# Kernel optimization log

Hardware: AMD Instinct MI355X
Metric: run time of the kernel (lower is better)

The kernel has to match this reference:

```python
import jax, jax.numpy as jnp
import numpy as np


def _maxpool2x2(x):
    # x: [N, C, H, W] -> [N, C, H//2, W//2]
    return jax.lax.reduce_window(x, -jnp.inf, jax.lax.max,
                                 (1, 1, 2, 2), (1, 1, 2, 2), 'VALID')


def _head(a, W1, b1, W2, b2, W3, b3):
    # headModel: maxpool -> (adaptive avgpool to 7x7 is identity here) -> flatten -> classifier (eval mode)
    mp = _maxpool2x2(a)                      # [N, 512, 7, 7]
    flat = mp.reshape(mp.shape[0], -1)       # [N, 25088]
    h = jax.nn.relu(flat @ W1.T + b1)        # [N, 4096]
    h = jax.nn.relu(h @ W2.T + b2)           # [N, 4096]
    return h @ W3.T + b3                     # [N, 1000]


def setup_inputs() -> dict:
    key = jax.random.key(0)
    ks = jax.random.split(key, 7)
    C, HW, FC, NC = 512, 14, 4096, 1000
    acts = jax.random.uniform(ks[0], (1, C, HW, HW), dtype=jnp.float32)  # post-ReLU feature map
    s1 = 1.0 / np.sqrt(C * 7 * 7)
    s2 = 1.0 / np.sqrt(FC)
    return {
        'activations': acts,
        'W1': jax.random.normal(ks[1], (FC, C * 7 * 7), dtype=jnp.float32) * s1,
        'b1': jax.random.normal(ks[2], (FC,), dtype=jnp.float32) * 0.01,
        'W2': jax.random.normal(ks[3], (FC, FC), dtype=jnp.float32) * s2,
        'b2': jax.random.normal(ks[4], (FC,), dtype=jnp.float32) * 0.01,
        'W3': jax.random.normal(ks[5], (NC, FC), dtype=jnp.float32) * s2,
        'b3': jax.random.normal(ks[6], (NC,), dtype=jnp.float32) * 0.01,
        'ht': 224,
        'wt': 224,
    }


def reference(activations, W1, b1, W2, b2, W3, b3, ht, wt):
    C = activations.shape[1]
    logits = _head(activations, W1, b1, W2, b2, W3, b3)   # [1, 1000]
    img_class = jnp.argmax(logits[0])
    base = logits[0, img_class]

    # Batch all C channel ablations: abl[i] = activations with channel i zeroed.
    mask = (1.0 - jnp.eye(C, dtype=activations.dtype))[:, :, None, None]  # [C, C, 1, 1]
    abl = activations * mask                                              # [C, C, 14, 14]
    logits_new = _head(abl, W1, b1, W2, b2, W3, b3)                        # [C, 1000]
    alpha = (base - jnp.take(logits_new, img_class, axis=1)) / base        # [C]

    # fused = relu(sum_i alpha_i * bilinear_resize(act_i)); resize is linear,
    # so weight in activation space and do one resize (same math as the loop).
    weighted = jnp.einsum('c,chw->hw', alpha, activations[0])              # [14, 14]
    sal = jax.image.resize(weighted[None, None], (1, 1, ht, wt),
                           method='bilinear')[0, 0]                        # [ht, wt]
    fused = jax.nn.relu(sal)
    mn, mx = fused.min(), fused.max()
    denom = jnp.where(mx != mn, mx - mn, 1.0)
    fused = jnp.where(mx != mn, (fused - mn) / denom, fused)
    return fused, img_class
```

## Files before the change

kernel.cpp:

```cpp
#include <hip/hip_runtime.h>
#include <math.h>

#define CCH 512
#define F1 25088
#define FC 4096
#define NCLS 1000
#define OW 224
#define KSPLIT 4
#define KSLICE 1024
#define PSTRIDE (CCH*FC)

#define WS_DT 0
#define WS_MP (WS_DT + FC*CCH)
#define WS_H1PRE (WS_MP + F1)
#define WS_H1 (WS_H1PRE + FC)
#define WS_H2 (WS_H1 + FC)
#define WS_H2PART (WS_H2 + FC)
#define WS_LOGITS (WS_H2PART + 4*FC)
#define WS_CLSBASE (WS_LOGITS + NCLS)
#define WS_ALPHA (WS_CLSBASE + 2)
#define WS_MINMAX (WS_ALPHA + CCH)
#define WS_LOGPART (WS_MINMAX + 2)
#define WS_A (WS_LOGPART + 64*CCH)
#define WS_PARTB (WS_A + CCH*FC/2)
#define WS_END (WS_PARTB + KSPLIT*CCH*FC/2)
#define WS_NEED_BYTES ((size_t)WS_END * 4)

typedef __attribute__((ext_vector_type(8))) short bfrag;
typedef __attribute__((ext_vector_type(4))) float f32x4;

static __device__ __forceinline__ unsigned short f2bf(float x) {
    unsigned u = __float_as_uint(x);
    unsigned r = 0x7FFFu + ((u >> 16) & 1u);
    return (unsigned short)((u + r) >> 16);
}

#define GLD16(g, l) __builtin_amdgcn_global_load_lds( \
    (const __attribute__((address_space(1))) void*)(g), \
    (__attribute__((address_space(3))) void*)(l), 16, 0, 0)

__global__ void k_maxpool(const float* __restrict__ act, float* __restrict__ ws) {
    int t = threadIdx.x;
    if (blockIdx.x == 0) {
        if (t == 0) ((int*)(ws + WS_MINMAX))[0] = 0x7F800000;
        if (t == 1) ((int*)(ws + WS_MINMAX))[1] = 0;
    }
    int idx = blockIdx.x * 256 + t;
    if (idx >= CCH * 49) return;
    int c = idx / 49, r = idx % 49, y = r / 7, x = r % 7;
    const float* a = act + c * 196 + (2 * y) * 14 + 2 * x;
    float m = fmaxf(fmaxf(a[0], a[1]), fmaxf(a[14], a[15]));
    ws[WS_MP + idx] = m;
}

__global__ __launch_bounds__(256) void k_phi5(const float* __restrict__ W1,
                                              const float* __restrict__ mp,
                                              const float* __restrict__ b1,
                                              float* __restrict__ Dt,
                                              float* __restrict__ h1pre,
                                              float* __restrict__ h1) {
    __shared__ float buf[12544];
    __shared__ float red[256];
    int j = blockIdx.x, t = threadIdx.x;
    const float* row = W1 + (size_t)j * F1;
    float sh[2];
    #pragma unroll
    for (int h = 0; h < 2; ++h) {
        __syncthreads();
        const float4* src = (const float4*)(row + h * 12544);
        const float4* msc = (const float4*)(mp + h * 12544);
        for (int n = t; n < 3136; n += 256) {
            float4 w = src[n], m = msc[n];
            float4 p;
            p.x = w.x * m.x; p.y = w.y * m.y; p.z = w.z * m.z; p.w = w.w * m.w;
            *(float4*)&buf[n * 4] = p;
        }
        __syncthreads();
        const float* bb = buf + t * 49;
        float s = 0.f;
        #pragma unroll
        for (int k = 0; k < 49; ++k) s += bb[k];
        Dt[(size_t)j * CCH + h * 256 + t] = s;
        sh[h] = s;
    }
    red[t] = sh[0] + sh[1];
    __syncthreads();
    if (t < 128) red[t] += red[t + 128];
    __syncthreads();
    if (t < 64) {
        float v = red[t] + red[t + 64];
        for (int off = 32; off > 0; off >>= 1) v += __shfl_down(v, off, 64);
        if (t == 0) { float hv = b1[j] + v; h1pre[j] = hv; h1[j] = fmaxf(hv, 0.f); }
    }
}

template <bool RELU>
__global__ void k_gemv4096(const float* __restrict__ M, const float* __restrict__ v,
                           const float* __restrict__ bias, float* __restrict__ out) {
    int j = blockIdx.x, t = threadIdx.x;
    const float4* row = (const float4*)(M + (size_t)j * FC);
    const float4* vv = (const float4*)v;
    float s = 0.f;
    #pragma unroll
    for (int q = 0; q < 4; ++q) {
        int n = q * 256 + t;
        float4 w = row[n], x = vv[n];
        s += w.x * x.x + w.y * x.y + w.z * x.z + w.w * x.w;
    }
    __shared__ float red[256];
    red[t] = s; __syncthreads();
    if (t < 128) red[t] += red[t + 128]; __syncthreads();
    if (t < 64)  red[t] += red[t + 64];  __syncthreads();
    if (t < 64) {
        float x = red[t];
        for (int off = 32; off > 0; off >>= 1) x += __shfl_down(x, off, 64);
        if (t == 0) { float r = bias[j] + x; out[j] = RELU ? fmaxf(r, 0.f) : r; }
    }
}

__global__ void k_argmax(const float* __restrict__ logits, float* __restrict__ clsbase,
                         float* __restrict__ dout_cls) {
    int t = threadIdx.x;
    float best = -INFINITY; int bi = NCLS;
    for (int n = t; n < NCLS; n += 256) {
        float v = logits[n];
        if (v > best || (v == best && n < bi)) { best = v; bi = n; }
    }
    __shared__ float bv[256]; __shared__ int bidx[256];
    bv[t] = best; bidx[t] = bi; __syncthreads();
    for (int o = 128; o > 0; o >>= 1) {
        if (t < o) {
            float v2 = bv[t + o]; int i2 = bidx[t + o];
            if (v2 > bv[t] || (v2 == bv[t] && i2 < bidx[t])) { bv[t] = v2; bidx[t] = i2; }
        }
        __syncthreads();
    }
    if (t == 0) { clsbase[0] = (float)bidx[0]; clsbase[1] = bv[0]; *dout_cls = (float)bidx[0]; }
}

__global__ __launch_bounds__(256) void k_abuild(const float* __restrict__ Dt,
                                                const float* __restrict__ h1pre,
                                                unsigned short* __restrict__ A) {
    __shared__ unsigned short tile[64][72];
    int kt = blockIdx.x, it = blockIdx.y, t = threadIdx.x;
    int k0 = kt * 64, i0 = it * 64;
    #pragma unroll
    for (int q = 0; q < 16; ++q) {
        int kk = q * 4 + (t >> 6);
        int ii = t & 63;
        float v = fmaxf(h1pre[k0 + kk] - Dt[(size_t)(k0 + kk) * CCH + i0 + ii], 0.f);
        tile[kk][ii] = f2bf(v);
    }
    __syncthreads();
    #pragma unroll
    for (int q = 0; q < 4; ++q) {
        int c = q * 256 + t;
        int ii = c >> 4, kc = c & 15;
        ushort4 v;
        v.x = tile[kc * 4 + 0][ii]; v.y = tile[kc * 4 + 1][ii];
        v.z = tile[kc * 4 + 2][ii]; v.w = tile[kc * 4 + 3][ii];
        *(ushort4*)&A[(size_t)(i0 + ii) * FC + k0 + kc * 4] = v;
    }
}

__global__ __launch_bounds__(256) void k_mfma_v4(
    const unsigned short* __restrict__ A, const float* __restrict__ W2,
    const float* __restrict__ h1, unsigned short* __restrict__ partb,
    float* __restrict__ h2part) {
    __shared__ char As[16384];
    __shared__ char Bs[16384];
    __shared__ float h1s[KSLICE];
    int nj = blockIdx.x;
    int mi = blockIdx.y;
    int ks = blockIdx.z;
    int t = threadIdx.x;
    int wid = t >> 6, lane = t & 63, lr = lane & 15, lh = lane >> 4;
    int i0 = mi * 128, j0 = nj * 128;
    int wr = (wid >> 1) * 64;
    int wc = (wid & 1) * 64;

    {
        float4 v = *(const float4*)(h1 + ks * KSLICE + t * 4);
        *(float4*)&h1s[t * 4] = v;
    }

    bool doh = (mi == 0);
    float hacc[4] = {0.f, 0.f, 0.f, 0.f};
    f32x4 acc[4][4];
    #pragma unroll
    for (int f = 0; f < 4; ++f)
        #pragma unroll
        for (int n = 0; n < 4; ++n) acc[f][n] = (f32x4){0.f, 0.f, 0.f, 0.f};

    for (int kst = 0; kst < KSLICE; kst += 64) {
        int k0 = ks * KSLICE + kst;
        __syncthreads();
        #pragma unroll
        for (int r = 0; r < 4; ++r) {
            int c = t + 256 * r;
            int row = c >> 3, ch = c & 7;
            GLD16(A + (size_t)(i0 + row) * FC + k0 + ((ch ^ (row & 7)) * 8),
                  As + (size_t)c * 16);
        }
        #pragma unroll
        for (int r = 0; r < 4; ++r) {
            int c = t + 256 * r;
            int row = c >> 3, ch = c & 7;
            int ko = (ch ^ (row & 7)) * 8;
            const float* wp = W2 + (size_t)(j0 + row) * FC + k0 + ko;
            float4 wa = *(const float4*)wp;
            float4 wb = *(const float4*)(wp + 4);
            if (doh) {
                hacc[r] += wa.x * h1s[kst + ko + 0] + wa.y * h1s[kst + ko + 1]
                         + wa.z * h1s[kst + ko + 2] + wa.w * h1s[kst + ko + 3]
                         + wb.x * h1s[kst + ko + 4] + wb.y * h1s[kst + ko + 5]
                         + wb.z * h1s[kst + ko + 6] + wb.w * h1s[kst + ko + 7];
            }
            union { bfrag v; unsigned short u[8]; } pk;
            pk.u[0] = f2bf(wa.x); pk.u[1] = f2bf(wa.y);
            pk.u[2] = f2bf(wa.z); pk.u[3] = f2bf(wa.w);
            pk.u[4] = f2bf(wb.x); pk.u[5] = f2bf(wb.y);
            pk.u[6] = f2bf(wb.z); pk.u[7] = f2bf(wb.w);
            *(bfrag*)(Bs + (size_t)c * 16) = pk.v;
        }
        __syncthreads();
        #pragma unroll
        for (int kf = 0; kf < 2; ++kf) {
            bfrag bv[4];
            #pragma unroll
            for (int n = 0; n < 4; ++n) {
                int br = wc + n * 16 + lr;
                bv[n] = *(const bfrag*)(Bs + ((size_t)br * 8 + ((kf * 4 + lh) ^ (br & 7))) * 16);
            }
            #pragma unroll
            for (int f = 0; f < 4; ++f) {
                int ar = wr + f * 16 + lr;
                bfrag av = *(const bfrag*)(As + ((size_t)ar * 8 + ((kf * 4 + lh) ^ (ar & 7))) * 16);
                #pragma unroll
                for (int n = 0; n < 4; ++n)
                    acc[f][n] = __builtin_amdgcn_mfma_f32_16x16x32_bf16(av, bv[n], acc[f][n], 0, 0, 0);
            }
        }
    }

    if (doh) {
        #pragma unroll
        for (int r = 0; r < 4; ++r) {
            float v = hacc[r];
            v += __shfl_down(v, 4, 8);
            v += __shfl_down(v, 2, 8);
            v += __shfl_down(v, 1, 8);
            if ((t & 7) == 0) h2part[ks * FC + j0 + r * 32 + (t >> 3)] = v;
        }
    }
    unsigned short* pb = partb + (size_t)ks * PSTRIDE;
    #pragma unroll
    for (int f = 0; f < 4; ++f) {
        int row0 = i0 + wr + f * 16 + lh * 4;
        #pragma unroll
        for (int rr = 0; rr < 4; ++rr) {
            #pragma unroll
            for (int n = 0; n < 4; ++n)
                pb[(size_t)(row0 + rr) * FC + j0 + wc + n * 16 + lr] = f2bf(acc[f][n][rr]);
        }
    }
}

__global__ void k_h2sum(const float* __restrict__ h2part, const float* __restrict__ b2,
                        float* __restrict__ h2) {
    int j = blockIdx.x * 256 + threadIdx.x;
    if (j < FC) {
        float v = b2[j] + ((h2part[j] + h2part[FC + j]) + (h2part[2 * FC + j] + h2part[3 * FC + j]));
        h2[j] = fmaxf(v, 0.f);
    }
}

__global__ __launch_bounds__(256) void k_alpha_b(
    const unsigned short* __restrict__ partb, const float* __restrict__ b2,
    const float* __restrict__ W3, const float* __restrict__ b3,
    const float* __restrict__ clsbase, float* __restrict__ alpha) {
    int i = blockIdx.x, t = threadIdx.x;
    int cls = (int)clsbase[0]; float base = clsbase[1];
    const float* w3r = W3 + (size_t)cls * FC;
    float s = 0.f;
    #pragma unroll
    for (int q = 0; q < 2; ++q) {
        int j = (q * 256 + t) * 8;
        uint4 p0 = *(const uint4*)(partb + (size_t)i * FC + j);
        uint4 p1 = *(const uint4*)(partb + (size_t)PSTRIDE + (size_t)i * FC + j);
        uint4 p2 = *(const uint4*)(partb + 2 * (size_t)PSTRIDE + (size_t)i * FC + j);
        uint4 p3 = *(const uint4*)(partb + 3 * (size_t)PSTRIDE + (size_t)i * FC + j);
        #pragma unroll
        for (int e = 0; e < 4; ++e) {
            unsigned a0 = ((const unsigned*)&p0)[e], a1 = ((const unsigned*)&p1)[e];
            unsigned a2 = ((const unsigned*)&p2)[e], a3 = ((const unsigned*)&p3)[e];
            float lo = (__uint_as_float(a0 << 16) + __uint_as_float(a1 << 16))
                     + (__uint_as_float(a2 << 16) + __uint_as_float(a3 << 16));
            float hi = (__uint_as_float(a0 & 0xFFFF0000u) + __uint_as_float(a1 & 0xFFFF0000u))
                     + (__uint_as_float(a2 & 0xFFFF0000u) + __uint_as_float(a3 & 0xFFFF0000u));
            int jj = j + e * 2;
            s += fmaxf(lo + b2[jj], 0.f) * w3r[jj];
            s += fmaxf(hi + b2[jj + 1], 0.f) * w3r[jj + 1];
        }
    }
    __shared__ float red[256];
    red[t] = s; __syncthreads();
    if (t < 128) red[t] += red[t + 128]; __syncthreads();
    if (t < 64)  red[t] += red[t + 64];  __syncthreads();
    if (t < 64) {
        float x = red[t];
        for (int off = 32; off > 0; off >>= 1) x += __shfl_down(x, off, 64);
        if (t == 0) alpha[i] = (base - (x + b3[cls])) / base;
    }
}

__global__ __launch_bounds__(256) void k_gemm_abl(
    const float* __restrict__ Dt, const float* __restrict__ h1pre,
    const float* __restrict__ W2, const float* __restrict__ b2,
    const float* __restrict__ W3, const float* __restrict__ clsbase,
    float* __restrict__ logit_part) {
    int mi = blockIdx.x, nj = blockIdx.y, t = threadIdx.x;
    int tx = t & 15, ty = t >> 4;
    int i0 = mi * 64, j0 = nj * 64;
    __shared__ float As2[16][64];
    __shared__ float Bs2[16][65];
    float acc[4][4] = {};
    for (int k0 = 0; k0 < FC; k0 += 16) {
        #pragma unroll
        for (int r = 0; r < 4; ++r) {
            int e = t + 256 * r; int kk = e >> 6, ii = e & 63;
            As2[kk][ii] = fmaxf(h1pre[k0 + kk] - Dt[(size_t)(k0 + kk) * CCH + i0 + ii], 0.f);
        }
        {
            int jj = t >> 2, kks = (t & 3) * 4;
            const float4 wv = *(const float4*)(W2 + (size_t)(j0 + jj) * FC + k0 + kks);
            Bs2[kks + 0][jj] = wv.x; Bs2[kks + 1][jj] = wv.y;
            Bs2[kks + 2][jj] = wv.z; Bs2[kks + 3][jj] = wv.w;
        }
        __syncthreads();
        #pragma unroll
        for (int kk = 0; kk < 16; ++kk) {
            float4 a4 = *(const float4*)&As2[kk][tx * 4];
            float av[4] = {a4.x, a4.y, a4.z, a4.w};
            float bv[4] = {Bs2[kk][ty * 4 + 0], Bs2[kk][ty * 4 + 1],
                           Bs2[kk][ty * 4 + 2], Bs2[kk][ty * 4 + 3]};
            #pragma unroll
            for (int a = 0; a < 4; ++a)
                #pragma unroll
                for (int b = 0; b < 4; ++b)
                    acc[a][b] = fmaf(av[a], bv[b], acc[a][b]);
        }
        __syncthreads();
    }
    int cls = (int)clsbase[0];
    const float* w3r = W3 + (size_t)cls * FC;
    float prt[4] = {0.f, 0.f, 0.f, 0.f};
    #pragma unroll
    for (int b = 0; b < 4; ++b) {
        int j2 = j0 + ty * 4 + b;
        float bb = b2[j2], w3 = w3r[j2];
        #pragma unroll
        for (int a = 0; a < 4; ++a) prt[a] = fmaf(fmaxf(acc[a][b] + bb, 0.f), w3, prt[a]);
    }
    __shared__ float red2[16][68];
    #pragma unroll
    for (int a = 0; a < 4; ++a) red2[ty][tx * 4 + a] = prt[a];
    __syncthreads();
    if (t < 64) {
        float s = 0.f;
        #pragma unroll
        for (int q = 0; q < 16; ++q) s += red2[q][t];
        logit_part[nj * CCH + i0 + t] = s;
    }
}

__global__ void k_alpha_fb(const float* __restrict__ logit_part, const float* __restrict__ b3,
                           const float* __restrict__ clsbase, float* __restrict__ alpha) {
    int t = blockIdx.x * 256 + threadIdx.x;
    if (t >= CCH) return;
    int cls = (int)clsbase[0]; float base = clsbase[1];
    float s = 0.f;
    for (int q = 0; q < 64; ++q) s += logit_part[q * CCH + t];
    alpha[t] = (base - (s + b3[cls])) / base;
}

__global__ void k_resize2(const float* __restrict__ alpha, const float* __restrict__ act,
                          float* __restrict__ out, int* __restrict__ minmax) {
    __shared__ float sA[CCH];
    __shared__ float sW[196];
    int t = threadIdx.x;
    for (int i = t; i < CCH; i += 256) sA[i] = alpha[i];
    __syncthreads();
    if (t < 196) {
        float s = 0.f;
        for (int c = 0; c < CCH; ++c) s = fmaf(sA[c], act[c * 196 + t], s);
        sW[t] = s;
    }
    __syncthreads();
    int pix = blockIdx.x * 256 + t;
    int y = pix / OW, x = pix % OW;
    float uy = (y + 0.5f) * 0.0625f - 0.5f;
    float ux = (x + 0.5f) * 0.0625f - 0.5f;
    float y0f = floorf(uy), x0f = floorf(ux);
    float fy = uy - y0f, fx = ux - x0f;
    int y0 = (int)y0f, x0 = (int)x0f;
    int y0c = min(max(y0, 0), 13), y1c = min(max(y0 + 1, 0), 13);
    int x0c = min(max(x0, 0), 13), x1c = min(max(x0 + 1, 0), 13);
    float v00 = sW[y0c * 14 + x0c], v01 = sW[y0c * 14 + x1c];
    float v10 = sW[y1c * 14 + x0c], v11 = sW[y1c * 14 + x1c];
    float v0 = v00 + (v01 - v00) * fx;
    float v1 = v10 + (v11 - v10) * fx;
    float v = v0 + (v1 - v0) * fy;
    float f = fmaxf(v, 0.f);
    out[pix] = f;
    __shared__ float rmn[256], rmx[256];
    rmn[t] = f; rmx[t] = f; __syncthreads();
    for (int o = 128; o > 0; o >>= 1) {
        if (t < o) { rmn[t] = fminf(rmn[t], rmn[t + o]); rmx[t] = fmaxf(rmx[t], rmx[t + o]); }
        __syncthreads();
    }
    if (t == 0) {
        atomicMin(&minmax[0], __float_as_int(rmn[0]));
        atomicMax(&minmax[1], __float_as_int(rmx[0]));
    }
}

__global__ void k_norm(float* __restrict__ out, const int* __restrict__ minmax) {
    float mn = __int_as_float(minmax[0]);
    float mx = __int_as_float(minmax[1]);
    int pix = blockIdx.x * 256 + threadIdx.x;
    if (mx != mn) out[pix] = (out[pix] - mn) / (mx - mn);
}

extern "C" void kernel_launch(void* const* d_in, const int* in_sizes, int n_in,
                              void* d_out, int out_size, void* d_ws, size_t ws_size,
                              hipStream_t stream) {
    const float* act = (const float*)d_in[0];
    const float* W1  = (const float*)d_in[1];
    const float* b1  = (const float*)d_in[2];
    const float* W2  = (const float*)d_in[3];
    const float* b2  = (const float*)d_in[4];
    const float* W3  = (const float*)d_in[5];
    const float* b3  = (const float*)d_in[6];
    float* out = (float*)d_out;
    float* ws = (float*)d_ws;
    const bool fast = (ws_size >= WS_NEED_BYTES);

    k_maxpool<<<98, 256, 0, stream>>>(act, ws);
    k_phi5<<<4096, 256, 0, stream>>>(W1, ws + WS_MP, b1, ws + WS_DT,
                                     ws + WS_H1PRE, ws + WS_H1);
    if (fast) {
        k_abuild<<<dim3(64, 8), 256, 0, stream>>>(ws + WS_DT, ws + WS_H1PRE,
                                                  (unsigned short*)(ws + WS_A));
        k_mfma_v4<<<dim3(32, 4, 4), 256, 0, stream>>>(
            (const unsigned short*)(ws + WS_A), W2, ws + WS_H1,
            (unsigned short*)(ws + WS_PARTB), ws + WS_H2PART);
        k_h2sum<<<16, 256, 0, stream>>>(ws + WS_H2PART, b2, ws + WS_H2);
        k_gemv4096<false><<<1000, 256, 0, stream>>>(W3, ws + WS_H2, b3, ws + WS_LOGITS);
        k_argmax<<<1, 256, 0, stream>>>(ws + WS_LOGITS, ws + WS_CLSBASE, out + 50176);
        k_alpha_b<<<CCH, 256, 0, stream>>>((const unsigned short*)(ws + WS_PARTB), b2,
                                           W3, b3, ws + WS_CLSBASE, ws + WS_ALPHA);
    } else {
        k_gemv4096<true><<<4096, 256, 0, stream>>>(W2, ws + WS_H1, b2, ws + WS_H2);
        k_gemv4096<false><<<1000, 256, 0, stream>>>(W3, ws + WS_H2, b3, ws + WS_LOGITS);
        k_argmax<<<1, 256, 0, stream>>>(ws + WS_LOGITS, ws + WS_CLSBASE, out + 50176);
        k_gemm_abl<<<dim3(8, 64), 256, 0, stream>>>(ws + WS_DT, ws + WS_H1PRE, W2, b2, W3,
                                                    ws + WS_CLSBASE, ws + WS_LOGPART);
        k_alpha_fb<<<2, 256, 0, stream>>>(ws + WS_LOGPART, b3, ws + WS_CLSBASE,
                                          ws + WS_ALPHA);
    }
    k_resize2<<<196, 256, 0, stream>>>(ws + WS_ALPHA, act, out, (int*)(ws + WS_MINMAX));
    k_norm<<<196, 256, 0, stream>>>(out, (const int*)(ws + WS_MINMAX));
}
```

Baseline: 224.3 us.

## Restructure ablation MFMA GEMM to read W2 once with deeper K split

The bf16 MFMA kernel now gives each 512-thread block all 512 ablation rows and a 64-column W2 slice over a 512-wide K slice, with eight K splits. Previously each W2 tile was loaded and converted once per 128-row M block, four times in total. W2 now streams from memory once, and the h2 GEMV work is spread evenly across blocks. The price is twice as many bf16 partial buffers to write and then re-read in the alpha reduction, plus a larger workspace. The W1 product kernel also batches six float4 loads per thread before use, to get more memory-level parallelism.

```diff
diff --git a/kernel.cpp b/kernel.cpp
--- a/kernel.cpp
+++ b/kernel.cpp
@@ -6,8 +6,8 @@
 #define FC 4096
 #define NCLS 1000
 #define OW 224
-#define KSPLIT 4
-#define KSLICE 1024
+#define KSPLIT 8
+#define KSL 512
 #define PSTRIDE (CCH*FC)
 
 #define WS_DT 0
@@ -16,7 +16,7 @@
 #define WS_H1 (WS_H1PRE + FC)
 #define WS_H2 (WS_H1 + FC)
 #define WS_H2PART (WS_H2 + FC)
-#define WS_LOGITS (WS_H2PART + 4*FC)
+#define WS_LOGITS (WS_H2PART + 8*FC)
 #define WS_CLSBASE (WS_LOGITS + NCLS)
 #define WS_ALPHA (WS_CLSBASE + 2)
 #define WS_MINMAX (WS_ALPHA + CCH)
@@ -53,7 +53,7 @@
     ws[WS_MP + idx] = m;
 }
 
-__global__ __launch_bounds__(256) void k_phi5(const float* __restrict__ W1,
+__global__ __launch_bounds__(256) void k_phi7(const float* __restrict__ W1,
                                               const float* __restrict__ mp,
                                               const float* __restrict__ b1,
                                               float* __restrict__ Dt,
@@ -62,14 +62,33 @@
     __shared__ float buf[12544];
     __shared__ float red[256];
     int j = blockIdx.x, t = threadIdx.x;
-    const float* row = W1 + (size_t)j * F1;
-    float sh[2];
+    const float4* wrow = (const float4*)(W1 + (size_t)j * F1);
+    const float4* mrow = (const float4*)mp;
+    float sh = 0.f;
     #pragma unroll
     for (int h = 0; h < 2; ++h) {
-        __syncthreads();
-        const float4* src = (const float4*)(row + h * 12544);
-        const float4* msc = (const float4*)(mp + h * 12544);
-        for (int n = t; n < 3136; n += 256) {
+        const float4* src = wrow + h * 3136;
+        const float4* msc = mrow + h * 3136;
+        __syncthreads();
+        #pragma unroll
+        for (int b = 0; b < 2; ++b) {
+            float4 w[6], m[6];
+            #pragma unroll
+            for (int e = 0; e < 6; ++e) {
+                int n = t + 256 * (b * 6 + e);
+                w[e] = src[n]; m[e] = msc[n];
+            }
+            #pragma unroll
+            for (int e = 0; e < 6; ++e) {
+                int n = t + 256 * (b * 6 + e);
+                float4 p;
+                p.x = w[e].x * m[e].x; p.y = w[e].y * m[e].y;
+                p.z = w[e].z * m[e].z; p.w = w[e].w * m[e].w;
+                *(float4*)&buf[n * 4] = p;
+            }
+        }
+        if (t < 64) {
+            int n = 3072 + t;
             float4 w = src[n], m = msc[n];
             float4 p;
             p.x = w.x * m.x; p.y = w.y * m.y; p.z = w.z * m.z; p.w = w.w * m.w;
@@ -81,9 +100,9 @@
         #pragma unroll
         for (int k = 0; k < 49; ++k) s += bb[k];
         Dt[(size_t)j * CCH + h * 256 + t] = s;
-        sh[h] = s;
-    }
-    red[t] = sh[0] + sh[1];
+        sh += s;
+    }
+    red[t] = sh;
     __syncthreads();
     if (t < 128) red[t] += red[t + 128];
     __syncthreads();
@@ -114,7 +133,7 @@
     if (t < 64) {
         float x = red[t];
         for (int off = 32; off > 0; off >>= 1) x += __shfl_down(x, off, 64);
-        if (t == 0) { float r = bias[j] + x; out[j] = RELU ? fmaxf(r, 0.f) : r; }
+        if (t == 0) { float r2 = bias[j] + x; out[j] = RELU ? fmaxf(r2, 0.f) : r2; }
     }
 }
 
@@ -163,105 +182,85 @@
     }
 }
 
-__global__ __launch_bounds__(256) void k_mfma_v4(
+__global__ __launch_bounds__(512) void k_mfma_v5(
     const unsigned short* __restrict__ A, const float* __restrict__ W2,
     const float* __restrict__ h1, unsigned short* __restrict__ partb,
     float* __restrict__ h2part) {
-    __shared__ char As[16384];
-    __shared__ char Bs[16384];
-    __shared__ float h1s[KSLICE];
-    int nj = blockIdx.x;
-    int mi = blockIdx.y;
-    int ks = blockIdx.z;
+    __shared__ char As[32768];
+    __shared__ char Bs[4096];
+    __shared__ float h1s[KSL];
+    int bid = blockIdx.x;
+    int ks = bid & 7, nj = bid >> 3;
     int t = threadIdx.x;
     int wid = t >> 6, lane = t & 63, lr = lane & 15, lh = lane >> 4;
-    int i0 = mi * 128, j0 = nj * 128;
-    int wr = (wid >> 1) * 64;
-    int wc = (wid & 1) * 64;
-
-    {
-        float4 v = *(const float4*)(h1 + ks * KSLICE + t * 4);
-        *(float4*)&h1s[t * 4] = v;
-    }
-
-    bool doh = (mi == 0);
-    float hacc[4] = {0.f, 0.f, 0.f, 0.f};
+    int j0 = nj * 64;
+    int kb = ks * KSL;
+
+    h1s[t] = h1[kb + t];
+
+    int brow = t >> 3, bkc = t & 7;
+    const float* wsrc = W2 + (size_t)(j0 + brow) * FC + kb + bkc * 4;
+    int bsw = (brow & 3) ^ ((brow >> 2) & 1);
+    char* bdst = Bs + ((size_t)(brow * 4) + ((bkc >> 1) ^ bsw)) * 16 + (bkc & 1) * 8;
+
+    float hacc = 0.f;
     f32x4 acc[4][4];
     #pragma unroll
     for (int f = 0; f < 4; ++f)
         #pragma unroll
         for (int n = 0; n < 4; ++n) acc[f][n] = (f32x4){0.f, 0.f, 0.f, 0.f};
 
-    for (int kst = 0; kst < KSLICE; kst += 64) {
-        int k0 = ks * KSLICE + kst;
+    for (int kst = 0; kst < KSL; kst += 32) {
         __syncthreads();
         #pragma unroll
         for (int r = 0; r < 4; ++r) {
-            int c = t + 256 * r;
-            int row = c >> 3, ch = c & 7;
-            GLD16(A + (size_t)(i0 + row) * FC + k0 + ((ch ^ (row & 7)) * 8),
+            int c = t + 512 * r;
+            int row = c >> 2, ch = c & 3;
+            int sw = (row & 3) ^ ((row >> 2) & 1);
+            GLD16(A + (size_t)row * FC + kb + kst + ((ch ^ sw) * 8),
                   As + (size_t)c * 16);
         }
-        #pragma unroll
-        for (int r = 0; r < 4; ++r) {
-            int c = t + 256 * r;
-            int row = c >> 3, ch = c & 7;
-            int ko = (ch ^ (row & 7)) * 8;
-            const float* wp = W2 + (size_t)(j0 + row) * FC + k0 + ko;
-            float4 wa = *(const float4*)wp;
-            float4 wb = *(const float4*)(wp + 4);
-            if (doh) {
-                hacc[r] += wa.x * h1s[kst + ko + 0] + wa.y * h1s[kst + ko + 1]
-                         + wa.z * h1s[kst + ko + 2] + wa.w * h1s[kst + ko + 3]
-                         + wb.x * h1s[kst + ko + 4] + wb.y * h1s[kst + ko + 5]
-                         + wb.z * h1s[kst + ko + 6] + wb.w * h1s[kst + ko + 7];
-            }
-            union { bfrag v; unsigned short u[8]; } pk;
-            pk.u[0] = f2bf(wa.x); pk.u[1] = f2bf(wa.y);
-            pk.u[2] = f2bf(wa.z); pk.u[3] = f2bf(wa.w);
-            pk.u[4] = f2bf(wb.x); pk.u[5] = f2bf(wb.y);
-            pk.u[6] = f2bf(wb.z); pk.u[7] = f2bf(wb.w);
-            *(bfrag*)(Bs + (size_t)c * 16) = pk.v;
-        }
-        __syncthreads();
-        #pragma unroll
-        for (int kf = 0; kf < 2; ++kf) {
-            bfrag bv[4];
-            #pragma unroll
-            for (int n = 0; n < 4; ++n) {
-                int br = wc + n * 16 + lr;
-                bv[n] = *(const bfrag*)(Bs + ((size_t)br * 8 + ((kf * 4 + lh) ^ (br & 7))) * 16);
-            }
-            #pragma unroll
-            for (int f = 0; f < 4; ++f) {
-                int ar = wr + f * 16 + lr;
-                bfrag av = *(const bfrag*)(As + ((size_t)ar * 8 + ((kf * 4 + lh) ^ (ar & 7))) * 16);
-                #pragma unroll
-                for (int n = 0; n < 4; ++n)
-                    acc[f][n] = __builtin_amdgcn_mfma_f32_16x16x32_bf16(av, bv[n], acc[f][n], 0, 0, 0);
-            }
-        }
-    }
-
-    if (doh) {
-        #pragma unroll
-        for (int r = 0; r < 4; ++r) {
-            float v = hacc[r];
-            v += __shfl_down(v, 4, 8);
-            v += __shfl_down(v, 2, 8);
-            v += __shfl_down(v, 1, 8);
-            if ((t & 7) == 0) h2part[ks * FC + j0 + r * 32 + (t >> 3)] = v;
-        }
-    }
+        {
+            float4 w = *(const float4*)(wsrc + kst);
+            hacc += w.x * h1s[kst + bkc * 4 + 0] + w.y * h1s[kst + bkc * 4 + 1]
+                  + w.z * h1s[kst + bkc * 4 + 2] + w.w * h1s[kst + bkc * 4 + 3];
+            ushort4 pk;
+            pk.x = f2bf(w.x); pk.y = f2bf(w.y); pk.z = f2bf(w.z); pk.w = f2bf(w.w);
+            *(ushort4*)bdst = pk;
+        }
+        __syncthreads();
+        bfrag bfr[4];
+        #pragma unroll
+        for (int n = 0; n < 4; ++n) {
+            int br = n * 16 + lr;
+            int swb = (br & 3) ^ ((br >> 2) & 1);
+            bfr[n] = *(const bfrag*)(Bs + ((size_t)(br * 4) + (lh ^ swb)) * 16);
+        }
+        #pragma unroll
+        for (int f = 0; f < 4; ++f) {
+            int ar = wid * 64 + f * 16 + lr;
+            int swa = (ar & 3) ^ ((ar >> 2) & 1);
+            bfrag av = *(const bfrag*)(As + ((size_t)(ar * 4) + (lh ^ swa)) * 16);
+            #pragma unroll
+            for (int n = 0; n < 4; ++n)
+                acc[f][n] = __builtin_amdgcn_mfma_f32_16x16x32_bf16(av, bfr[n], acc[f][n], 0, 0, 0);
+        }
+    }
+
+    hacc += __shfl_down(hacc, 4, 8);
+    hacc += __shfl_down(hacc, 2, 8);
+    hacc += __shfl_down(hacc, 1, 8);
+    if (bkc == 0) h2part[ks * FC + j0 + brow] = hacc;
+
     unsigned short* pb = partb + (size_t)ks * PSTRIDE;
     #pragma unroll
     for (int f = 0; f < 4; ++f) {
-        int row0 = i0 + wr + f * 16 + lh * 4;
+        int row0 = wid * 64 + f * 16 + lh * 4;
         #pragma unroll
         for (int rr = 0; rr < 4; ++rr) {
             #pragma unroll
             for (int n = 0; n < 4; ++n)
-                pb[(size_t)(row0 + rr) * FC + j0 + wc + n * 16 + lr] = f2bf(acc[f][n][rr]);
+                pb[(size_t)(row0 + rr) * FC + j0 + n * 16 + lr] = f2bf(acc[f][n][rr]);
         }
     }
 }
@@ -270,7 +269,9 @@
                         float* __restrict__ h2) {
     int j = blockIdx.x * 256 + threadIdx.x;
     if (j < FC) {
-        float v = b2[j] + ((h2part[j] + h2part[FC + j]) + (h2part[2 * FC + j] + h2part[3 * FC + j]));
+        float v = b2[j];
+        #pragma unroll
+        for (int p = 0; p < KSPLIT; ++p) v += h2part[p * FC + j];
         h2[j] = fmaxf(v, 0.f);
     }
 }
@@ -285,23 +286,23 @@
     float s = 0.f;
     #pragma unroll
     for (int q = 0; q < 2; ++q) {
-        int j = (q * 256 + t) * 8;
-        uint4 p0 = *(const uint4*)(partb + (size_t)i * FC + j);
-        uint4 p1 = *(const uint4*)(partb + (size_t)PSTRIDE + (size_t)i * FC + j);
-        uint4 p2 = *(const uint4*)(partb + 2 * (size_t)PSTRIDE + (size_t)i * FC + j);
-        uint4 p3 = *(const uint4*)(partb + 3 * (size_t)PSTRIDE + (size_t)i * FC + j);
-        #pragma unroll
-        for (int e = 0; e < 4; ++e) {
-            unsigned a0 = ((const unsigned*)&p0)[e], a1 = ((const unsigned*)&p1)[e];
-            unsigned a2 = ((const unsigned*)&p2)[e], a3 = ((const unsigned*)&p3)[e];
-            float lo = (__uint_as_float(a0 << 16) + __uint_as_float(a1 << 16))
-                     + (__uint_as_float(a2 << 16) + __uint_as_float(a3 << 16));
-            float hi = (__uint_as_float(a0 & 0xFFFF0000u) + __uint_as_float(a1 & 0xFFFF0000u))
-                     + (__uint_as_float(a2 & 0xFFFF0000u) + __uint_as_float(a3 & 0xFFFF0000u));
-            int jj = j + e * 2;
-            s += fmaxf(lo + b2[jj], 0.f) * w3r[jj];
-            s += fmaxf(hi + b2[jj + 1], 0.f) * w3r[jj + 1];
-        }
+        int jj = (q * 256 + t) * 8;
+        float acc8[8];
+        #pragma unroll
+        for (int e = 0; e < 8; ++e) acc8[e] = b2[jj + e];
+        #pragma unroll
+        for (int p = 0; p < KSPLIT; ++p) {
+            uint4 pv = *(const uint4*)(partb + (size_t)p * PSTRIDE + (size_t)i * FC + jj);
+            #pragma unroll
+            for (int e = 0; e < 4; ++e) {
+                unsigned a = ((const unsigned*)&pv)[e];
+                acc8[e * 2]     += __uint_as_float(a << 16);
+                acc8[e * 2 + 1] += __uint_as_float(a & 0xFFFF0000u);
+            }
+        }
+        #pragma unroll
+        for (int e = 0; e < 8; ++e)
+            s += fmaxf(acc8[e], 0.f) * w3r[jj + e];
     }
     __shared__ float red[256];
     red[t] = s; __syncthreads();
@@ -447,12 +448,12 @@
     const bool fast = (ws_size >= WS_NEED_BYTES);
 
     k_maxpool<<<98, 256, 0, stream>>>(act, ws);
-    k_phi5<<<4096, 256, 0, stream>>>(W1, ws + WS_MP, b1, ws + WS_DT,
+    k_phi7<<<4096, 256, 0, stream>>>(W1, ws + WS_MP, b1, ws + WS_DT,
                                      ws + WS_H1PRE, ws + WS_H1);
     if (fast) {
         k_abuild<<<dim3(64, 8), 256, 0, stream>>>(ws + WS_DT, ws + WS_H1PRE,
                                                   (unsigned short*)(ws + WS_A));
-        k_mfma_v4<<<dim3(32, 4, 4), 256, 0, stream>>>(
+        k_mfma_v5<<<512, 512, 0, stream>>>(
             (const unsigned short*)(ws + WS_A), W2, ws + WS_H1,
             (unsigned short*)(ws + WS_PARTB), ws + WS_H2PART);
         k_h2sum<<<16, 256, 0, stream>>>(ws + WS_H2PART, b2, ws + WS_H2);
```

Measured after the change: 210.1 us. 6.4% less time.
